# Optimization experiments

Hardware: AMD Instinct MI355X
Metric: run time of the kernel (lower is better)

The kernel has to match this reference:

```python
import jax, jax.numpy as jnp
import numpy as np

DECAY = 0.99
EPS = 1e-05


def setup_inputs() -> dict:
    key = jax.random.key(0)
    k1, k2 = jax.random.split(key)
    B, T, D, K = 16, 4096, 256, 1024
    z = jax.random.normal(k1, (B, T, D), dtype=jnp.float32)
    embedding = jax.random.normal(k2, (D, K), dtype=jnp.float32)
    cluster_size = jnp.zeros((K,), dtype=jnp.float32)
    embedding_mean = embedding.copy()  # torch init: embedding.clone()
    return {"z": z, "embedding": embedding, "cluster_size": cluster_size,
            "embedding_mean": embedding_mean}


def reference(z, embedding, cluster_size, embedding_mean):
    """Training-mode forward of CodebookEMA (proj=False).

    z:              [B, T, D]
    embedding:      [D, K] codebook buffer
    cluster_size:   [K]    EMA cluster counts
    embedding_mean: [D, K] EMA cluster sums
    Returns (z_q, commitment_loss, codebook_loss, code,
             new_embedding, new_cluster_size, new_embedding_mean).
    """
    B, T, D = z.shape
    K = embedding.shape[1]
    z_flat = z.reshape(B * T, D)

    # squared-distance quantization: ||z||^2 - 2 z.E + ||e||^2  -> [BT, K]
    dist = ((z_flat * z_flat).sum(1, keepdims=True)
            - 2.0 * (z_flat @ embedding)
            + (embedding * embedding).sum(0)[None, :])
    idx = jnp.argmin(dist, axis=1)              # [BT]
    code = idx.reshape(B, T)

    # EMA codebook update (no one-hot materialization; use segment sums)
    counts = jax.ops.segment_sum(jnp.ones_like(idx, dtype=z.dtype), idx,
                                 num_segments=K)               # [K]
    emb_sum = jax.ops.segment_sum(z_flat, idx, num_segments=K).T  # [D, K]
    new_cluster_size = cluster_size * DECAY + (1.0 - DECAY) * counts
    new_embedding_mean = embedding_mean * DECAY + (1.0 - DECAY) * emb_sum
    n = new_cluster_size.sum()
    cs_norm = (new_cluster_size + EPS) / (n + K * EPS) * n     # Laplace-smoothed
    new_embedding = new_embedding_mean / cs_norm[None, :]      # [D, K]

    # dequantize with the *updated* codebook (as in the torch control flow)
    z_q = new_embedding.T[code]                                # [B, T, D]

    commitment_loss = ((jax.lax.stop_gradient(z_q) - z) ** 2).mean(axis=(1, 2))
    codebook_loss = jnp.zeros((B,), dtype=z.dtype)
    z_q = z + jax.lax.stop_gradient(z_q - z)  # straight-through estimator
    return (z_q, commitment_loss, codebook_loss, code,
            new_embedding, new_cluster_size, new_embedding_mean)
```

## Files before the change

### kernel.cpp

```cpp
#include <hip/hip_runtime.h>
#include <cfloat>
#include <climits>
#include <cstdint>

#define B_ 16
#define T_ 4096
#define D_ 256
#define K_ 1024
#define BT_ 65536
#define DECAYF 0.99f
#define OMDECAYF 0.01f
#define EPSF 1e-5f
#define TAUGAP 0.125f
#define CHUNK 32
#define GROUP 16
#define RMARGIN 0.01f

typedef float f32x4 __attribute__((ext_vector_type(4)));
typedef _Float16 f16x8 __attribute__((ext_vector_type(8)));

__device__ __forceinline__ void gload16(const void* g, void* l) {
    __builtin_amdgcn_global_load_lds(
        (const __attribute__((address_space(1))) void*)g,
        (__attribute__((address_space(3))) void*)l, 16, 0, 0);
}

__global__ void k_prep(const float* __restrict__ z, const float* __restrict__ E,
                       _Float16* __restrict__ zf, _Float16* __restrict__ EfT,
                       float* __restrict__ enorm, double* __restrict__ enorm64,
                       int* __restrict__ counts, int* __restrict__ nflag,
                       float* __restrict__ out_closs, float* __restrict__ out_cbl,
                       float* __restrict__ emb_sum) {
    int b = blockIdx.x;
    if (b < 8192) {
        int base = (b * 256 + threadIdx.x) * 8;
        float4 v0 = *(const float4*)(z + base);
        float4 v1 = *(const float4*)(z + base + 4);
        f16x8 h;
        h[0] = (_Float16)v0.x; h[1] = (_Float16)v0.y;
        h[2] = (_Float16)v0.z; h[3] = (_Float16)v0.w;
        h[4] = (_Float16)v1.x; h[5] = (_Float16)v1.y;
        h[6] = (_Float16)v1.z; h[7] = (_Float16)v1.w;
        *(f16x8*)(zf + base) = h;
    } else {
        __shared__ double rd[256];
        int n = b - 8192, d = threadIdx.x;
        float v = E[(size_t)d * K_ + n];
        EfT[(size_t)n * 256 + d] = (_Float16)v;
        rd[d] = (double)v * (double)v;
        __syncthreads();
        for (int st = 128; st > 0; st >>= 1) {
            if (d < st) rd[d] += rd[d + st];
            __syncthreads();
        }
        if (d == 0) { enorm[n] = (float)rd[0]; enorm64[n] = rd[0]; }
        emb_sum[(size_t)n * 256 + d] = 0.f;
        if (n < 4) counts[n * 256 + d] = 0;
        if (n == 4) {
            if (d < 16) out_closs[d] = 0.f;
            else if (d < 32) out_cbl[d - 16] = 0.f;
            else if (d == 32) *nflag = 0;
        }
    }
}

__global__ __launch_bounds__(512, 2) void k_argmin_mfma(
    const _Float16* __restrict__ zf, const _Float16* __restrict__ EfT,
    const float* __restrict__ enorm, int* __restrict__ code,
    int* __restrict__ flags, int* __restrict__ nflag, int* __restrict__ counts) {
    __shared__ _Float16 Ab[2][128 * 32];
    __shared__ _Float16 Bb[2][256 * 32];

    const int t = threadIdx.x;
    const int row0 = blockIdx.x * 128;
    const int l = t & 63, wid = t >> 6;
    const int wr = wid >> 2, wc = wid & 3;
    const int lr = l & 15, lk = l >> 4;

    const int arow = t >> 2,          ablk = (t & 3) ^ ((arow >> 1) & 3);
    const int brow0 = t >> 2,         bblk0 = (t & 3) ^ ((brow0 >> 1) & 3);
    const int brow1 = (t + 512) >> 2, bblk1 = ((t + 512) & 3) ^ ((brow1 >> 1) & 3);

#define STAGE(it_, buf_) do {                                                       \
        int nc_ = (it_) >> 3; int kb_ = ((it_) & 7) * 32;                            \
        gload16(zf + (size_t)(row0 + arow) * 256 + kb_ + ablk * 8,                   \
                &Ab[buf_][(t & ~63) * 8]);                                           \
        gload16(EfT + (size_t)(nc_ * 256 + brow0) * 256 + kb_ + bblk0 * 8,           \
                &Bb[buf_][(t & ~63) * 8]);                                           \
        gload16(EfT + (size_t)(nc_ * 256 + brow1) * 256 + kb_ + bblk1 * 8,           \
                &Bb[buf_][((t + 512) & ~63) * 8]);                                   \
    } while (0)

    STAGE(0, 0);

    float D1[4][4], D2[4][4];
    int   I1[4][4];
    #pragma unroll
    for (int m = 0; m < 4; ++m)
        #pragma unroll
        for (int r = 0; r < 4; ++r) {
            D1[m][r] = FLT_MAX; D2[m][r] = FLT_MAX; I1[m][r] = 0x7fffffff;
        }

    f32x4 acc[4][4];
    for (int it = 0; it < 32; ++it) {
        if ((it & 7) == 0) {
            #pragma unroll
            for (int m = 0; m < 4; ++m)
                #pragma unroll
                for (int n = 0; n < 4; ++n) acc[m][n] = (f32x4){0.f, 0.f, 0.f, 0.f};
        }
        __syncthreads();
        if (it + 1 < 32) STAGE(it + 1, (it + 1) & 1);
        const _Float16* Abuf = Ab[it & 1];
        const _Float16* Bbuf = Bb[it & 1];
        f16x8 a[4], b[4];
        #pragma unroll
        for (int m = 0; m < 4; ++m) {
            int row = wr * 64 + m * 16 + lr;
            a[m] = *(const f16x8*)&Abuf[row * 32 + ((lk ^ ((row >> 1) & 3)) * 8)];
        }
        #pragma unroll
        for (int n = 0; n < 4; ++n) {
            int nn = wc * 64 + n * 16 + lr;
            b[n] = *(const f16x8*)&Bbuf[nn * 32 + ((lk ^ ((nn >> 1) & 3)) * 8)];
        }
        #pragma unroll
        for (int m = 0; m < 4; ++m)
            #pragma unroll
            for (int n = 0; n < 4; ++n)
                acc[m][n] = __builtin_amdgcn_mfma_f32_16x16x32_f16(
                    a[m], b[n], acc[m][n], 0, 0, 0);

        if ((it & 7) == 7) {
            int nc = it >> 3;
            float en[4];
            #pragma unroll
            for (int n = 0; n < 4; ++n)
                en[n] = enorm[nc * 256 + wc * 64 + n * 16 + lr];
            #pragma unroll
            for (int m = 0; m < 4; ++m)
                #pragma unroll
                for (int r = 0; r < 4; ++r)
                    #pragma unroll
                    for (int n = 0; n < 4; ++n) {
                        float dist = en[n] - 2.0f * acc[m][n][r];
                        int cg = nc * 256 + wc * 64 + n * 16 + lr;
                        if (dist < D1[m][r]) {
                            D2[m][r] = D1[m][r]; D1[m][r] = dist; I1[m][r] = cg;
                        } else D2[m][r] = fminf(D2[m][r], dist);
                    }
        }
    }
#undef STAGE

    __syncthreads();
    float* mg_d1 = (float*)&Ab[0][0];
    int*   mg_i1 = (int*)(mg_d1 + 512);
    float* mg_d2 = (float*)(mg_i1 + 512);

    #pragma unroll
    for (int m = 0; m < 4; ++m)
        #pragma unroll
        for (int r = 0; r < 4; ++r) {
            float d1 = D1[m][r], d2 = D2[m][r];
            int i1 = I1[m][r];
            #pragma unroll
            for (int mask = 1; mask < 16; mask <<= 1) {
                float pd1 = __shfl_xor(d1, mask);
                int   pi1 = __shfl_xor(i1, mask);
                float pd2 = __shfl_xor(d2, mask);
                if (pd1 < d1 || (pd1 == d1 && pi1 < i1)) {
                    d2 = fminf(d1, pd2); d1 = pd1; i1 = pi1;
                } else d2 = fminf(d2, pd1);
            }
            if (lr == 0) {
                int row = wr * 64 + m * 16 + lk * 4 + r;
                mg_d1[row * 4 + wc] = d1;
                mg_i1[row * 4 + wc] = i1;
                mg_d2[row * 4 + wc] = d2;
            }
        }
    __syncthreads();
    if (t < 128) {
        float b1 = FLT_MAX, b2 = FLT_MAX;
        int bi = 0x7fffffff;
        #pragma unroll
        for (int c = 0; c < 4; ++c) {
            float pd1 = mg_d1[t * 4 + c];
            int   pi1 = mg_i1[t * 4 + c];
            float pd2 = mg_d2[t * 4 + c];
            if (pd1 < b1 || (pd1 == b1 && pi1 < bi)) {
                b2 = fminf(b1, pd2); b1 = pd1; bi = pi1;
            } else b2 = fminf(b2, pd1);
        }
        code[row0 + t] = bi;
        atomicAdd(&counts[bi], 1);
        if (b2 - b1 < TAUGAP) {
            int pos = atomicAdd(nflag, 1);
            flags[pos] = row0 + t;
        }
    }
}

__global__ __launch_bounds__(256) void k_fixup(
    const float* __restrict__ z, const float* __restrict__ E,
    const float* __restrict__ enorm, const double* __restrict__ enorm64,
    const int* __restrict__ nflag, const int* __restrict__ flags,
    int* __restrict__ code, int* __restrict__ counts) {
    __shared__ float  zrows[GROUP][256];
    __shared__ int    rowid[GROUP];
    __shared__ float  bw[GROUP][4];
    __shared__ float  bestAll[GROUP];
    __shared__ int    ccnt[GROUP];
    __shared__ int    cand[GROUP][16];
    __shared__ double cdist[GROUP][16];

    const int t = threadIdx.x, w = t >> 6, l = t & 63;
    const int n = *nflag;
    const int ngroups = (n + GROUP - 1) / GROUP;

    for (int g = blockIdx.x; g < ngroups; g += gridDim.x) {
        __syncthreads();
        if (t < GROUP) {
            int idx = g * GROUP + t;
            rowid[t] = (idx < n) ? flags[idx] : -1;
            ccnt[t] = 0;
        }
        __syncthreads();
        {
            int i = t >> 4, s = t & 15;
            int r = rowid[i];
            const float* src = z + (size_t)(r < 0 ? 0 : r) * D_ + s * 16;
            float4 a0 = *(const float4*)(src + 0);
            float4 a1 = *(const float4*)(src + 4);
            float4 a2 = *(const float4*)(src + 8);
            float4 a3 = *(const float4*)(src + 12);
            *(float4*)&zrows[i][s * 16 + 0]  = a0;
            *(float4*)&zrows[i][s * 16 + 4]  = a1;
            *(float4*)&zrows[i][s * 16 + 8]  = a2;
            *(float4*)&zrows[i][s * 16 + 12] = a3;
        }
        __syncthreads();

        float acc[GROUP][4];
        #pragma unroll
        for (int i = 0; i < GROUP; ++i) {
            acc[i][0] = 0.f; acc[i][1] = 0.f; acc[i][2] = 0.f; acc[i][3] = 0.f;
        }
        const float* Ecol = E + 4 * t;
        for (int d = 0; d < D_; ++d) {
            float4 ev = *(const float4*)(Ecol + (size_t)d * K_);
            #pragma unroll
            for (int i = 0; i < GROUP; ++i) {
                float zd = zrows[i][d];
                acc[i][0] = fmaf(zd, ev.x, acc[i][0]);
                acc[i][1] = fmaf(zd, ev.y, acc[i][1]);
                acc[i][2] = fmaf(zd, ev.z, acc[i][2]);
                acc[i][3] = fmaf(zd, ev.w, acc[i][3]);
            }
        }
        float en0 = enorm[4 * t], en1 = enorm[4 * t + 1];
        float en2 = enorm[4 * t + 2], en3 = enorm[4 * t + 3];
        #pragma unroll
        for (int i = 0; i < GROUP; ++i) {
            acc[i][0] = en0 - 2.f * acc[i][0];
            acc[i][1] = en1 - 2.f * acc[i][1];
            acc[i][2] = en2 - 2.f * acc[i][2];
            acc[i][3] = en3 - 2.f * acc[i][3];
        }
        #pragma unroll
        for (int i = 0; i < GROUP; ++i) {
            float b = fminf(fminf(acc[i][0], acc[i][1]), fminf(acc[i][2], acc[i][3]));
            #pragma unroll
            for (int m = 1; m < 64; m <<= 1) b = fminf(b, __shfl_xor(b, m));
            if (l == 0) bw[i][w] = b;
        }
        __syncthreads();
        if (t < GROUP)
            bestAll[t] = fminf(fminf(bw[t][0], bw[t][1]), fminf(bw[t][2], bw[t][3]));
        __syncthreads();
        #pragma unroll
        for (int i = 0; i < GROUP; ++i) {
            float thr = bestAll[i] + RMARGIN;
            #pragma unroll
            for (int j = 0; j < 4; ++j) {
                if (acc[i][j] <= thr) {
                    int slot = atomicAdd(&ccnt[i], 1);
                    if (slot < 16) cand[i][slot] = 4 * t + j;
                }
            }
        }
        __syncthreads();
        for (int p = w; p < GROUP * 16; p += 4) {
            int i = p >> 4, s = p & 15;
            int cn = ccnt[i];
            if (rowid[i] < 0 || cn < 2 || s >= (cn < 16 ? cn : 16)) continue;
            int c = cand[i][s];
            double dot = 0.0;
            #pragma unroll
            for (int q = 0; q < 4; ++q) {
                int d = l * 4 + q;
                dot = fma((double)zrows[i][d], (double)E[(size_t)d * K_ + c], dot);
            }
            #pragma unroll
            for (int m = 1; m < 64; m <<= 1) dot += __shfl_xor(dot, m);
            if (l == 0) cdist[i][s] = enorm64[c] - 2.0 * dot;
        }
        __syncthreads();
        if (t < GROUP) {
            int r = rowid[t];
            if (r >= 0) {
                int cn = ccnt[t]; if (cn > 16) cn = 16;
                int newc;
                if (cn <= 1) {
                    newc = cand[t][0];
                } else {
                    double bd = DBL_MAX; int bi = INT_MAX;
                    for (int s = 0; s < cn; ++s) {
                        double dv = cdist[t][s]; int ci = cand[t][s];
                        if (dv < bd || (dv == bd && ci < bi)) { bd = dv; bi = ci; }
                    }
                    newc = bi;
                }
                int oldc = code[r];
                if (newc != oldc) {
                    code[r] = newc;
                    atomicSub(&counts[oldc], 1);
                    atomicAdd(&counts[newc], 1);
                }
            }
        }
    }
}

__global__ void k_scan(const int* __restrict__ counts, const float* __restrict__ cs,
                       int* __restrict__ offsets, int* __restrict__ cursor,
                       float* __restrict__ out_newcs, float* __restrict__ csnorm,
                       int* __restrict__ work, int* __restrict__ nwork) {
    __shared__ int   s[K_];
    __shared__ int   c[K_];
    __shared__ float red[K_];
    int t = threadIdx.x;
    int v = counts[t];
    int nch = (v + CHUNK - 1) / CHUNK;
    s[t] = v;
    c[t] = nch;
    float ncs = cs[t] * DECAYF + OMDECAYF * (float)v;
    out_newcs[t] = ncs;
    red[t] = ncs;
    __syncthreads();
    for (int d = 1; d < K_; d <<= 1) {
        int x = (t >= d) ? s[t - d] : 0;
        int y = (t >= d) ? c[t - d] : 0;
        __syncthreads();
        s[t] += x; c[t] += y;
        __syncthreads();
    }
    offsets[t] = s[t] - v;
    cursor[t]  = s[t] - v;
    if (t == K_ - 1) { offsets[K_] = s[t]; *nwork = c[t]; }
    int wbase = c[t] - nch;
    for (int j = 0; j < nch; ++j) work[wbase + j] = (t << 16) | j;
    for (int st = 512; st > 0; st >>= 1) {
        if (t < st) red[t] += red[t + st];
        __syncthreads();
    }
    float nsum = red[0];
    csnorm[t] = (ncs + EPSF) / (nsum + (float)K_ * EPSF) * nsum;
}

__global__ void k_sortidx(const int* __restrict__ code, int* __restrict__ cursor,
                          int* __restrict__ sorted) {
    int r = blockIdx.x * 256 + threadIdx.x;
    int cc = code[r];
    int pos = atomicAdd(&cursor[cc], 1);
    sorted[pos] = r;
}

__global__ void k_segsum(const float* __restrict__ z, const int* __restrict__ sorted,
                         const int* __restrict__ offsets, const int* __restrict__ work,
                         const int* __restrict__ nwork, float* __restrict__ emb_sum) {
    int NW = *nwork;
    int d = threadIdx.x;
    for (int i = blockIdx.x; i < NW; i += gridDim.x) {
        int wk = work[i];
        int k = wk >> 16, j = wk & 0xffff;
        int beg = offsets[k] + j * CHUNK;
        int end = min(beg + CHUNK, offsets[k + 1]);
        float s = 0.f;
        int idx = beg;
        for (; idx + 8 <= end; idx += 8) {
            int r0 = sorted[idx],     r1 = sorted[idx + 1];
            int r2 = sorted[idx + 2], r3 = sorted[idx + 3];
            int r4 = sorted[idx + 4], r5 = sorted[idx + 5];
            int r6 = sorted[idx + 6], r7 = sorted[idx + 7];
            float v0 = z[(size_t)r0 * D_ + d];
            float v1 = z[(size_t)r1 * D_ + d];
            float v2 = z[(size_t)r2 * D_ + d];
            float v3 = z[(size_t)r3 * D_ + d];
            float v4 = z[(size_t)r4 * D_ + d];
            float v5 = z[(size_t)r5 * D_ + d];
            float v6 = z[(size_t)r6 * D_ + d];
            float v7 = z[(size_t)r7 * D_ + d];
            s += ((v0 + v1) + (v2 + v3)) + ((v4 + v5) + (v6 + v7));
        }
        for (; idx < end; ++idx) s += z[(size_t)sorted[idx] * D_ + d];
        atomicAdd(&emb_sum[(size_t)k * D_ + d], s);
    }
}

__global__ void k_emb(const float* __restrict__ EM, const float* __restrict__ emb_sum,
                      const float* __restrict__ csnorm,
                      float* __restrict__ out_newemb, float* __restrict__ out_newem,
                      float* __restrict__ newembT) {
    int tid = blockIdx.x * 256 + threadIdx.x;
    int k = tid >> 8, d = tid & 255;
    float em  = EM[(size_t)d * K_ + k];
    float nem = em * DECAYF + OMDECAYF * emb_sum[tid];
    float nq  = nem / csnorm[k];
    out_newem [(size_t)d * K_ + k] = nem;
    out_newemb[(size_t)d * K_ + k] = nq;
    newembT[tid] = nq;
}

__global__ __launch_bounds__(256) void k_gather(
    const float* __restrict__ z, const int* __restrict__ code,
    const float* __restrict__ newembT,
    float* __restrict__ out_zq, float* __restrict__ out_code,
    float* __restrict__ out_closs) {
    __shared__ double wsum[4];
    const int w = threadIdx.x >> 6, l = threadIdx.x & 63;
    const int base = blockIdx.x * 32 + w * 8;
    int i0 = code[base],     i1 = code[base + 1], i2 = code[base + 2], i3 = code[base + 3];
    int i4 = code[base + 4], i5 = code[base + 5], i6 = code[base + 6], i7 = code[base + 7];
    float4 z0 = *(const float4*)(z + (size_t)(base    ) * D_ + l * 4);
    float4 z1 = *(const float4*)(z + (size_t)(base + 1) * D_ + l * 4);
    float4 z2 = *(const float4*)(z + (size_t)(base + 2) * D_ + l * 4);
    float4 z3 = *(const float4*)(z + (size_t)(base + 3) * D_ + l * 4);
    float4 z4 = *(const float4*)(z + (size_t)(base + 4) * D_ + l * 4);
    float4 z5 = *(const float4*)(z + (size_t)(base + 5) * D_ + l * 4);
    float4 z6 = *(const float4*)(z + (size_t)(base + 6) * D_ + l * 4);
    float4 z7 = *(const float4*)(z + (size_t)(base + 7) * D_ + l * 4);
    float4 e0 = *(const float4*)(newembT + (size_t)i0 * D_ + l * 4);
    float4 e1 = *(const float4*)(newembT + (size_t)i1 * D_ + l * 4);
    float4 e2 = *(const float4*)(newembT + (size_t)i2 * D_ + l * 4);
    float4 e3 = *(const float4*)(newembT + (size_t)i3 * D_ + l * 4);
    float4 e4 = *(const float4*)(newembT + (size_t)i4 * D_ + l * 4);
    float4 e5 = *(const float4*)(newembT + (size_t)i5 * D_ + l * 4);
    float4 e6 = *(const float4*)(newembT + (size_t)i6 * D_ + l * 4);
    float4 e7 = *(const float4*)(newembT + (size_t)i7 * D_ + l * 4);
    *(float4*)(out_zq + (size_t)(base    ) * D_ + l * 4) = e0;
    *(float4*)(out_zq + (size_t)(base + 1) * D_ + l * 4) = e1;
    *(float4*)(out_zq + (size_t)(base + 2) * D_ + l * 4) = e2;
    *(float4*)(out_zq + (size_t)(base + 3) * D_ + l * 4) = e3;
    *(float4*)(out_zq + (size_t)(base + 4) * D_ + l * 4) = e4;
    *(float4*)(out_zq + (size_t)(base + 5) * D_ + l * 4) = e5;
    *(float4*)(out_zq + (size_t)(base + 6) * D_ + l * 4) = e6;
    *(float4*)(out_zq + (size_t)(base + 7) * D_ + l * 4) = e7;
    if (l == 0) {
        out_code[base]     = (float)i0; out_code[base + 1] = (float)i1;
        out_code[base + 2] = (float)i2; out_code[base + 3] = (float)i3;
        out_code[base + 4] = (float)i4; out_code[base + 5] = (float)i5;
        out_code[base + 6] = (float)i6; out_code[base + 7] = (float)i7;
    }
    double acc = 0.0;
    float dx, dy, dz2, dw2;
    dx = e0.x - z0.x; dy = e0.y - z0.y; dz2 = e0.z - z0.z; dw2 = e0.w - z0.w;
    acc += (double)dx * dx + (double)dy * dy + (double)dz2 * dz2 + (double)dw2 * dw2;
    dx = e1.x - z1.x; dy = e1.y - z1.y; dz2 = e1.z - z1.z; dw2 = e1.w - z1.w;
    acc += (double)dx * dx + (double)dy * dy + (double)dz2 * dz2 + (double)dw2 * dw2;
    dx = e2.x - z2.x; dy = e2.y - z2.y; dz2 = e2.z - z2.z; dw2 = e2.w - z2.w;
    acc += (double)dx * dx + (double)dy * dy + (double)dz2 * dz2 + (double)dw2 * dw2;
    dx = e3.x - z3.x; dy = e3.y - z3.y; dz2 = e3.z - z3.z; dw2 = e3.w - z3.w;
    acc += (double)dx * dx + (double)dy * dy + (double)dz2 * dz2 + (double)dw2 * dw2;
    dx = e4.x - z4.x; dy = e4.y - z4.y; dz2 = e4.z - z4.z; dw2 = e4.w - z4.w;
    acc += (double)dx * dx + (double)dy * dy + (double)dz2 * dz2 + (double)dw2 * dw2;
    dx = e5.x - z5.x; dy = e5.y - z5.y; dz2 = e5.z - z5.z; dw2 = e5.w - z5.w;
    acc += (double)dx * dx + (double)dy * dy + (double)dz2 * dz2 + (double)dw2 * dw2;
    dx = e6.x - z6.x; dy = e6.y - z6.y; dz2 = e6.z - z6.z; dw2 = e6.w - z6.w;
    acc += (double)dx * dx + (double)dy * dy + (double)dz2 * dz2 + (double)dw2 * dw2;
    dx = e7.x - z7.x; dy = e7.y - z7.y; dz2 = e7.z - z7.z; dw2 = e7.w - z7.w;
    acc += (double)dx * dx + (double)dy * dy + (double)dz2 * dz2 + (double)dw2 * dw2;
    #pragma unroll
    for (int off = 32; off > 0; off >>= 1) acc += __shfl_down(acc, off);
    if (l == 0) wsum[w] = acc;
    __syncthreads();
    if (threadIdx.x == 0) {
        float v = (float)((wsum[0] + wsum[1] + wsum[2] + wsum[3]) *
                          (1.0 / ((double)T_ * (double)D_)));
        atomicAdd(&out_closs[blockIdx.x >> 7], v);
    }
}

extern "C" void kernel_launch(void* const* d_in, const int* in_sizes, int n_in,
                              void* d_out, int out_size, void* d_ws, size_t ws_size,
                              hipStream_t stream) {
    (void)in_sizes; (void)n_in; (void)out_size; (void)ws_size;
    const float* z  = (const float*)d_in[0];
    const float* E  = (const float*)d_in[1];
    const float* cs = (const float*)d_in[2];
    const float* EM = (const float*)d_in[3];

    float* out       = (float*)d_out;
    float* out_zq    = out;
    float* out_closs = out + 16777216;
    float* out_cbl   = out_closs + 16;
    float* out_code  = out_cbl + 16;
    float* out_nemb  = out_code + 65536;
    float* out_ncs   = out_nemb + 262144;
    float* out_nem   = out_ncs + 1024;

    _Float16* zf = (_Float16*)out_zq;

    char* w = (char*)d_ws;
    int*      counts  = (int*)(w + 0);
    int*      nflag   = (int*)(w + 4096);
    int*      offsets = (int*)(w + 4160);
    int*      cursor  = (int*)(w + 8320);
    float*    enorm   = (float*)(w + 12416);
    int*      code_i  = (int*)(w + 16512);
    int*      flags   = (int*)(w + 278656);
    float*    csnorm  = (float*)(w + 540800);
    float*    newembT = (float*)(w + 544896);
    _Float16* EfT     = (_Float16*)(w + 1593472);
    int*      sorted  = (int*)(w + 2117760);
    float*    emb_sum = (float*)(w + 2379904);
    int*      work    = (int*)(w + 3428480);
    int*      nwork   = (int*)(w + 3444864);
    double*   enorm64 = (double*)(w + 3444928);

    k_prep       <<<9216, 256, 0, stream>>>(z, E, zf, EfT, enorm, enorm64, counts,
                                            nflag, out_closs, out_cbl, emb_sum);
    k_argmin_mfma<<<BT_ / 128, 512, 0, stream>>>(zf, EfT, enorm, code_i, flags,
                                                 nflag, counts);
    k_fixup      <<<256, 256, 0, stream>>>(z, E, enorm, enorm64, nflag, flags,
                                           code_i, counts);
    k_scan       <<<1, K_, 0, stream>>>(counts, cs, offsets, cursor, out_ncs, csnorm,
                                        work, nwork);
    k_sortidx    <<<BT_ / 256, 256, 0, stream>>>(code_i, cursor, sorted);
    k_segsum     <<<2048, 256, 0, stream>>>(z, sorted, offsets, work, nwork, emb_sum);
    k_emb        <<<(K_ * D_) / 256, 256, 0, stream>>>(EM, emb_sum, csnorm,
                                                       out_nemb, out_nem, newembT);
    k_gather     <<<BT_ / 32, 256, 0, stream>>>(z, code_i, newembT, out_zq, out_code,
                                                out_closs);
}
```

Baseline: 286.7 us.

## Keep full z tile resident in LDS and stream codebook from global

```diff
diff --git a/kernel.cpp b/kernel.cpp
--- a/kernel.cpp
+++ b/kernel.cpp
@@ -68,8 +68,7 @@
     const _Float16* __restrict__ zf, const _Float16* __restrict__ EfT,
     const float* __restrict__ enorm, int* __restrict__ code,
     int* __restrict__ flags, int* __restrict__ nflag, int* __restrict__ counts) {
-    __shared__ _Float16 Ab[2][128 * 32];
-    __shared__ _Float16 Bb[2][256 * 32];
+    __shared__ _Float16 At[128 * 256];
 
     const int t = threadIdx.x;
     const int row0 = blockIdx.x * 128;
@@ -77,21 +76,15 @@
     const int wr = wid >> 2, wc = wid & 3;
     const int lr = l & 15, lk = l >> 4;
 
-    const int arow = t >> 2,          ablk = (t & 3) ^ ((arow >> 1) & 3);
-    const int brow0 = t >> 2,         bblk0 = (t & 3) ^ ((brow0 >> 1) & 3);
-    const int brow1 = (t + 512) >> 2, bblk1 = ((t + 512) & 3) ^ ((brow1 >> 1) & 3);
-
-#define STAGE(it_, buf_) do {                                                       \
-        int nc_ = (it_) >> 3; int kb_ = ((it_) & 7) * 32;                            \
-        gload16(zf + (size_t)(row0 + arow) * 256 + kb_ + ablk * 8,                   \
-                &Ab[buf_][(t & ~63) * 8]);                                           \
-        gload16(EfT + (size_t)(nc_ * 256 + brow0) * 256 + kb_ + bblk0 * 8,           \
-                &Bb[buf_][(t & ~63) * 8]);                                           \
-        gload16(EfT + (size_t)(nc_ * 256 + brow1) * 256 + kb_ + bblk1 * 8,           \
-                &Bb[buf_][((t + 512) & ~63) * 8]);                                   \
-    } while (0)
-
-    STAGE(0, 0);
+    #pragma unroll
+    for (int j = 0; j < 8; ++j) {
+        int slot = j * 512 + t;
+        int arow = slot >> 5, ablk = slot & 31;
+        gload16(zf + (size_t)(row0 + arow) * 256 + ((ablk ^ (arow & 7)) * 8),
+                &At[(size_t)(j * 512 + (t & ~63)) * 8]);
+    }
+    asm volatile("s_waitcnt vmcnt(0)" ::: "memory");
+    __syncthreads();
 
     float D1[4][4], D2[4][4];
     int   I1[4][4];
@@ -102,60 +95,55 @@
             D1[m][r] = FLT_MAX; D2[m][r] = FLT_MAX; I1[m][r] = 0x7fffffff;
         }
 
-    f32x4 acc[4][4];
-    for (int it = 0; it < 32; ++it) {
-        if ((it & 7) == 0) {
+    const _Float16* bbase = EfT + (size_t)(wc * 64 + lr) * 256 + lk * 8;
+
+    for (int nc = 0; nc < 4; ++nc) {
+        f32x4 acc[4][4];
+        #pragma unroll
+        for (int m = 0; m < 4; ++m)
+            #pragma unroll
+            for (int n = 0; n < 4; ++n) acc[m][n] = (f32x4){0.f, 0.f, 0.f, 0.f};
+
+        const _Float16* bp = bbase + (size_t)nc * 256 * 256;
+        #pragma unroll
+        for (int ks = 0; ks < 8; ++ks) {
+            f16x8 a[4], b[4];
+            #pragma unroll
+            for (int n = 0; n < 4; ++n)
+                b[n] = *(const f16x8*)(bp + n * 16 * 256 + ks * 32);
+            #pragma unroll
+            for (int m = 0; m < 4; ++m) {
+                int row = wr * 64 + m * 16 + lr;
+                a[m] = *(const f16x8*)&At[row * 256 + (((ks * 4 + lk) ^ (row & 7)) * 8)];
+            }
             #pragma unroll
             for (int m = 0; m < 4; ++m)
                 #pragma unroll
-                for (int n = 0; n < 4; ++n) acc[m][n] = (f32x4){0.f, 0.f, 0.f, 0.f};
-        }
-        __syncthreads();
-        if (it + 1 < 32) STAGE(it + 1, (it + 1) & 1);
-        const _Float16* Abuf = Ab[it & 1];
-        const _Float16* Bbuf = Bb[it & 1];
-        f16x8 a[4], b[4];
-        #pragma unroll
-        for (int m = 0; m < 4; ++m) {
-            int row = wr * 64 + m * 16 + lr;
-            a[m] = *(const f16x8*)&Abuf[row * 32 + ((lk ^ ((row >> 1) & 3)) * 8)];
-        }
-        #pragma unroll
-        for (int n = 0; n < 4; ++n) {
-            int nn = wc * 64 + n * 16 + lr;
-            b[n] = *(const f16x8*)&Bbuf[nn * 32 + ((lk ^ ((nn >> 1) & 3)) * 8)];
-        }
+                for (int n = 0; n < 4; ++n)
+                    acc[m][n] = __builtin_amdgcn_mfma_f32_16x16x32_f16(
+                        a[m], b[n], acc[m][n], 0, 0, 0);
+        }
+
+        float en[4];
+        #pragma unroll
+        for (int n = 0; n < 4; ++n)
+            en[n] = enorm[nc * 256 + wc * 64 + n * 16 + lr];
         #pragma unroll
         for (int m = 0; m < 4; ++m)
             #pragma unroll
-            for (int n = 0; n < 4; ++n)
-                acc[m][n] = __builtin_amdgcn_mfma_f32_16x16x32_f16(
-                    a[m], b[n], acc[m][n], 0, 0, 0);
-
-        if ((it & 7) == 7) {
-            int nc = it >> 3;
-            float en[4];
-            #pragma unroll
-            for (int n = 0; n < 4; ++n)
-                en[n] = enorm[nc * 256 + wc * 64 + n * 16 + lr];
-            #pragma unroll
-            for (int m = 0; m < 4; ++m)
+            for (int r = 0; r < 4; ++r)
                 #pragma unroll
-                for (int r = 0; r < 4; ++r)
-                    #pragma unroll
-                    for (int n = 0; n < 4; ++n) {
-                        float dist = en[n] - 2.0f * acc[m][n][r];
-                        int cg = nc * 256 + wc * 64 + n * 16 + lr;
-                        if (dist < D1[m][r]) {
-                            D2[m][r] = D1[m][r]; D1[m][r] = dist; I1[m][r] = cg;
-                        } else D2[m][r] = fminf(D2[m][r], dist);
-                    }
-        }
-    }
-#undef STAGE
+                for (int n = 0; n < 4; ++n) {
+                    float dist = en[n] - 2.0f * acc[m][n][r];
+                    int cg = nc * 256 + wc * 64 + n * 16 + lr;
+                    if (dist < D1[m][r]) {
+                        D2[m][r] = D1[m][r]; D1[m][r] = dist; I1[m][r] = cg;
+                    } else D2[m][r] = fminf(D2[m][r], dist);
+                }
+    }
 
     __syncthreads();
-    float* mg_d1 = (float*)&Ab[0][0];
+    float* mg_d1 = (float*)&At[0];
     int*   mg_i1 = (int*)(mg_d1 + 512);
     float* mg_d2 = (float*)(mg_i1 + 512);
 
```

After: 320.1 us. +11.7%, slower.
